# Optimization experiments

Measured on AMD Instinct MI355X. Metric: run time of the kernel, lower is better.

## Reference

```python
import jax, jax.numpy as jnp
import numpy as np

B, C, H, W = 2, 256, 64, 64  # C = in_channels; x has 2*C channels
DQ = C // 16


def setup_inputs() -> dict:
    key = jax.random.key(0)
    ks = jax.random.split(key, 10)
    s = 0.05
    return {
        "x": jax.random.normal(ks[0], (B, 2 * C, H, W), dtype=jnp.float32),
        "Wq": jax.random.normal(ks[1], (DQ, C), dtype=jnp.float32) * s,
        "bq": jax.random.normal(ks[2], (DQ,), dtype=jnp.float32) * s,
        "Wk": jax.random.normal(ks[3], (DQ, C), dtype=jnp.float32) * s,
        "bk": jax.random.normal(ks[4], (DQ,), dtype=jnp.float32) * s,
        "Wv": jax.random.normal(ks[5], (C, C), dtype=jnp.float32) * s,
        "bv": jax.random.normal(ks[6], (C,), dtype=jnp.float32) * s,
        "Wpt": jax.random.normal(ks[7], (C, 2 * C), dtype=jnp.float32) * s,
        "bpt": jax.random.normal(ks[8], (C,), dtype=jnp.float32) * s,
        "gamma": jnp.full((1,), 0.5, dtype=jnp.float32),  # original inits to 0; nonzero for a non-trivial output
    }


def _conv1x1(x, Wt, b):
    # 1x1 conv == per-pixel linear map over channels
    return jnp.einsum("bchw,dc->bdhw", x, Wt) + b[None, :, None, None]


def reference(x, Wq, bq, Wk, bk, Wv, bv, Wpt, bpt, gamma):
    n = x.shape[1] // 2
    x1, x2 = x[:, :n], x[:, n:]
    b, c, h, w = x1.shape
    hw = h * w

    def qkv(xi):
        q = _conv1x1(xi, Wq, bq).reshape(b, DQ, hw)   # [B,dq,HW]
        k = _conv1x1(xi, Wk, bk).reshape(b, DQ, hw)   # [B,dq,HW]
        v = _conv1x1(xi, Wv, bv).reshape(b, c, hw)    # [B,C,HW]
        return q, k, v

    q1, k1, v1 = qkv(x1)
    q2, k2, v2 = qkv(x2)

    # attn[b,i,j] = softmax_j( q[:,i] . k[:,j] )  (no scaling, as in original)
    attn1 = jax.nn.softmax(jnp.einsum("bdi,bdj->bij", q1, k1), axis=-1)  # [B,HW,HW]
    attn2 = jax.nn.softmax(jnp.einsum("bdi,bdj->bij", q2, k2), axis=-1)

    def apply_attn(v, attn):
        # out[b,c,i] = sum_j v[b,c,j] * attn[b,i,j]
        return jnp.einsum("bcj,bij->bci", v, attn).reshape(b, c, h, w)

    out11 = apply_attn(v1, attn1)
    out12 = apply_attn(v2, attn1)
    out21 = apply_attn(v1, attn2)
    out22 = apply_attn(v2, attn2)

    o1 = _conv1x1(jnp.concatenate([out11, out12], axis=1), Wpt, bpt)  # [B,C,H,W]
    o2 = _conv1x1(jnp.concatenate([out21, out22], axis=1), Wpt, bpt)

    out = gamma * jnp.concatenate([o1, o2], axis=1) + x
    return out
```

## Files before the change

### kernel.cpp

```cpp
#include <hip/hip_runtime.h>
#include <hip/hip_bf16.h>


#define HW 4096
#define CC 256
#define DQ 16

typedef __hip_bfloat16 bf16;
struct alignas(8) bh4 { bf16 x, y, z, w; };
typedef __bf16 bf16x8 __attribute__((ext_vector_type(8)));
typedef float  f32x4  __attribute__((ext_vector_type(4)));

static __device__ __forceinline__ float b2f(bf16 v) { return __bfloat162float(v); }
static __device__ __forceinline__ float ldf(const void* p, size_t i, bool isb) {
    return isb ? b2f(((const bf16*)p)[i]) : ((const float*)p)[i];
}

static __device__ __forceinline__ void load_lds16(const void* g, void* l) {
    __builtin_amdgcn_global_load_lds(
        (const __attribute__((address_space(1))) unsigned int*)g,
        (__attribute__((address_space(3))) unsigned int*)l, 16, 0, 0);
}

__global__ void __launch_bounds__(256)
prep_w(const void* __restrict__ Wq_r, const void* __restrict__ bq_r,
       const void* __restrict__ Wk_r, const void* __restrict__ bk_r,
       const void* __restrict__ Wv_r, const void* __restrict__ bv_r,
       const void* __restrict__ Wpt_r, const void* __restrict__ bpt_r,
       const void* __restrict__ gam_r,
       float* __restrict__ bqf, float* __restrict__ bkf, float* __restrict__ gamf,
       bf16* __restrict__ Wqb, bf16* __restrict__ Wkb,
       bf16* __restrict__ McB, float* __restrict__ btot,
       const unsigned short* __restrict__ probe) {
    int bx = blockIdx.x, tid = threadIdx.x;
    bool isb = probe[0] != 0;
    if (bx < 512) {
        int d = bx >> 1;
        int c = ((bx & 1) << 8) + tid;
        int half = c >> 8, cm = c & 255;
        size_t wp = (size_t)d * 512 + half * 256;
        float a0 = 0.f, a1 = 0.f, a2 = 0.f, a3 = 0.f;
        if (isb) {
            const bf16* Wp = (const bf16*)Wpt_r + wp;
            const bf16* Wv = (const bf16*)Wv_r + cm;
#pragma unroll 8
            for (int e = 0; e < 256; e += 4) {
                a0 = fmaf(b2f(Wp[e + 0]), b2f(Wv[(size_t)(e + 0) * 256]), a0);
                a1 = fmaf(b2f(Wp[e + 1]), b2f(Wv[(size_t)(e + 1) * 256]), a1);
                a2 = fmaf(b2f(Wp[e + 2]), b2f(Wv[(size_t)(e + 2) * 256]), a2);
                a3 = fmaf(b2f(Wp[e + 3]), b2f(Wv[(size_t)(e + 3) * 256]), a3);
            }
        } else {
            const float* Wp = (const float*)Wpt_r + wp;
            const float* Wv = (const float*)Wv_r + cm;
#pragma unroll 8
            for (int e = 0; e < 256; e += 4) {
                a0 = fmaf(Wp[e + 0], Wv[(size_t)(e + 0) * 256], a0);
                a1 = fmaf(Wp[e + 1], Wv[(size_t)(e + 1) * 256], a1);
                a2 = fmaf(Wp[e + 2], Wv[(size_t)(e + 2) * 256], a2);
                a3 = fmaf(Wp[e + 3], Wv[(size_t)(e + 3) * 256], a3);
            }
        }
        McB[d * 512 + c] = __float2bfloat16((a0 + a1) + (a2 + a3));
    } else if (bx == 512) {
        int d = tid;
        float a0 = 0.f, a1 = 0.f, a2 = 0.f, a3 = 0.f;
#pragma unroll 8
        for (int e = 0; e < 256; e += 4) {
            a0 = fmaf(ldf(Wpt_r, (size_t)d * 512 + e + 0, isb) + ldf(Wpt_r, (size_t)d * 512 + 256 + e + 0, isb), ldf(bv_r, e + 0, isb), a0);
            a1 = fmaf(ldf(Wpt_r, (size_t)d * 512 + e + 1, isb) + ldf(Wpt_r, (size_t)d * 512 + 256 + e + 1, isb), ldf(bv_r, e + 1, isb), a1);
            a2 = fmaf(ldf(Wpt_r, (size_t)d * 512 + e + 2, isb) + ldf(Wpt_r, (size_t)d * 512 + 256 + e + 2, isb), ldf(bv_r, e + 2, isb), a2);
            a3 = fmaf(ldf(Wpt_r, (size_t)d * 512 + e + 3, isb) + ldf(Wpt_r, (size_t)d * 512 + 256 + e + 3, isb), ldf(bv_r, e + 3, isb), a3);
        }
        btot[d] = ldf(bpt_r, d, isb) + ((a0 + a1) + (a2 + a3));
    } else if (bx < 545) {
        int id = bx - 513;
        const void* s = id < 16 ? Wq_r : Wk_r;
        bf16* dst = id < 16 ? Wqb : Wkb;
        int i = (id & 15) * 256 + tid;
        dst[i] = __float2bfloat16(ldf(s, i, isb));
    } else {
        if (tid < 16) bqf[tid] = ldf(bq_r, tid, isb);
        else if (tid < 32) bkf[tid - 16] = ldf(bk_r, tid - 16, isb);
        else if (tid == 32) gamf[0] = ldf(gam_r, 0, isb);
    }
}

__global__ void __launch_bounds__(256)
prep_x(const void* __restrict__ xsrc, bf16* __restrict__ Xt,
       const unsigned short* __restrict__ probe) {
    __shared__ float T[64][65];
    int id = blockIdx.x, tid = threadIdx.x;
    bool isb = probe[0] != 0;
    int j0 = (id & 63) * 64, e0 = ((id >> 6) & 7) * 64, b = id >> 9;
    int j_l = tid & 63, er0 = (tid >> 6) * 16;
#pragma unroll
    for (int r = 0; r < 16; ++r) {
        size_t src = ((size_t)(b * 512 + e0 + er0 + r)) * HW + j0 + j_l;
        T[er0 + r][j_l] = ldf(xsrc, src, isb);
    }
    __syncthreads();
    int e_w = tid & 63, jr0 = (tid >> 6) * 16;
#pragma unroll
    for (int r = 0; r < 16; ++r)
        Xt[((size_t)b * HW + j0 + jr0 + r) * 512 + e0 + e_w] =
            __float2bfloat16(T[e_w][jr0 + r]);
}

__global__ void __launch_bounds__(256, 2)
qku(const bf16* __restrict__ Xt,
    const bf16* __restrict__ Wqb, const float* __restrict__ bqf,
    const bf16* __restrict__ Wkb, const float* __restrict__ bkf,
    bf16* __restrict__ Qb, bf16* __restrict__ Kb,
    const bf16* __restrict__ McB, bf16* __restrict__ Ub) {
    __shared__ __align__(16) bf16 sA[64 * 64];
    __shared__ __align__(16) bf16 sB[128 * 64];
    int tid = threadIdx.x;
    int lane = tid & 63, wave = tid >> 6;
    int ln = lane & 15, q = lane >> 4;
    int bx = blockIdx.x;

    if (bx < 256) {
        int bh = bx >> 6;
        int b = bh >> 1, h = bh & 1;
        int j0 = (bx & 63) * 64 + wave * 16;
        bf16x8 aQ[8], aK[8];
#pragma unroll
        for (int kk = 0; kk < 8; ++kk) {
            aQ[kk] = *(const bf16x8*)&Wqb[ln * 256 + kk * 32 + q * 8];
            aK[kk] = *(const bf16x8*)&Wkb[ln * 256 + kk * 32 + q * 8];
        }
        const bf16* Xrow = Xt + ((size_t)b * HW + j0 + ln) * 512 + h * 256;
        f32x4 dQ = {0.f, 0.f, 0.f, 0.f}, dK = {0.f, 0.f, 0.f, 0.f};
#pragma unroll
        for (int kk = 0; kk < 8; ++kk) {
            bf16x8 bxv = *(const bf16x8*)&Xrow[kk * 32 + q * 8];
            dQ = __builtin_amdgcn_mfma_f32_16x16x32_bf16(aQ[kk], bxv, dQ, 0, 0, 0);
            dK = __builtin_amdgcn_mfma_f32_16x16x32_bf16(aK[kk], bxv, dK, 0, 0, 0);
        }
        size_t rowoff = ((size_t)bh * HW + j0 + ln) * 32;
        bh4 oq, ok;
        oq.x = __float2bfloat16(dQ[0] + bqf[q * 4 + 0]);
        oq.y = __float2bfloat16(dQ[1] + bqf[q * 4 + 1]);
        oq.z = __float2bfloat16(dQ[2] + bqf[q * 4 + 2]);
        oq.w = __float2bfloat16(dQ[3] + bqf[q * 4 + 3]);
        ok.x = __float2bfloat16(dK[0] + bkf[q * 4 + 0]);
        ok.y = __float2bfloat16(dK[1] + bkf[q * 4 + 1]);
        ok.z = __float2bfloat16(dK[2] + bkf[q * 4 + 2]);
        ok.w = __float2bfloat16(dK[3] + bkf[q * 4 + 3]);
        bh4 z; z.x = z.y = z.z = z.w = __float2bfloat16(0.f);
        *(bh4*)&Qb[rowoff + q * 4] = oq;
        *(bh4*)&Qb[rowoff + 16 + q * 4] = z;
        *(bh4*)&Kb[rowoff + q * 4] = ok;
        *(bh4*)&Kb[rowoff + 16 + q * 4] = z;
        return;
    }

    int id = bx - 256;
    int wm = (wave >> 1) * 32, wn = (wave & 1) * 64;
    int j0 = (id & 31) * 128, c0 = ((id >> 5) & 3) * 64, b = id >> 7;
    const bf16* Xb = Xt + (size_t)b * HW * 512;
    f32x4 acc[2][4];
#pragma unroll
    for (int mi = 0; mi < 2; ++mi)
#pragma unroll
        for (int ni = 0; ni < 4; ++ni)
#pragma unroll
            for (int r = 0; r < 4; ++r) acc[mi][ni][r] = 0.f;

    for (int e0 = 0; e0 < 512; e0 += 64) {
        __syncthreads();
#pragma unroll
        for (int r = 0; r < 2; ++r) {
            int s = r * 256 + tid;
            int row = s >> 3, jc = s & 7, jg = jc ^ (row & 7);
            load_lds16(McB + (size_t)(c0 + row) * 512 + e0 + jg * 8, sA + s * 8);
        }
#pragma unroll
        for (int r = 0; r < 4; ++r) {
            int s = r * 256 + tid;
            int row = s >> 3, jc = s & 7, jg = jc ^ (row & 7);
            load_lds16(Xb + (size_t)(j0 + row) * 512 + e0 + jg * 8, sB + s * 8);
        }
        __syncthreads();
#pragma unroll
        for (int kh = 0; kh < 2; ++kh) {
            bf16x8 af[2], bfv[4];
#pragma unroll
            for (int mi = 0; mi < 2; ++mi) {
                int row = wm + mi * 16 + ln;
                int jc = (kh * 4 + q) ^ (row & 7);
                af[mi] = *(const bf16x8*)&sA[row * 64 + jc * 8];
            }
#pragma unroll
            for (int ni = 0; ni < 4; ++ni) {
                int row = wn + ni * 16 + ln;
                int jc = (kh * 4 + q) ^ (row & 7);
                bfv[ni] = *(const bf16x8*)&sB[row * 64 + jc * 8];
            }
#pragma unroll
            for (int mi = 0; mi < 2; ++mi)
#pragma unroll
                for (int ni = 0; ni < 4; ++ni)
                    acc[mi][ni] = __builtin_amdgcn_mfma_f32_16x16x32_bf16(
                        af[mi], bfv[ni], acc[mi][ni], 0, 0, 0);
        }
    }
#pragma unroll
    for (int mi = 0; mi < 2; ++mi)
#pragma unroll
        for (int r = 0; r < 4; ++r) {
            int c = c0 + wm + mi * 16 + q * 4 + r;
#pragma unroll
            for (int ni = 0; ni < 4; ++ni) {
                int j = j0 + wn + ni * 16 + ln;
                Ub[((size_t)(b * CC + c)) * HW + j] = __float2bfloat16(acc[mi][ni][r]);
            }
        }
}

__global__ void __launch_bounds__(256, 4)
flash_attn(const bf16* __restrict__ Ub, const bf16* __restrict__ Qb,
           const bf16* __restrict__ Kb, const float* __restrict__ btot,
           const void* __restrict__ xorig, const float* __restrict__ gamf,
           void* __restrict__ outv, const unsigned short* __restrict__ probe) {
    __shared__ __align__(16) bf16 sU[2][128 * 64];
    __shared__ __align__(16) bf16 sE[32 * 64];
    __shared__ float sL[2][32];
    int tid  = threadIdx.x;
    int lane = tid & 63, wave = tid >> 6;
    int ln = lane & 15, q = lane >> 4;
    int iw = wave & 1, jw = wave >> 1;

    int bid = blockIdx.x;
    int panel = bid & 7;
    int i0 = (bid >> 3) * 32;
    int c0 = (panel & 1) * 128;
    int bh = panel >> 1;
    int b = bh >> 1, h = bh & 1;

    const bf16* Ubb = Ub + (size_t)b * CC * HW + (size_t)c0 * HW;
    const bf16* Kbh = Kb + (size_t)bh * HW * 32;

    bf16x8 bq = *(const bf16x8*)&Qb[((size_t)bh * HW + i0 + iw * 16 + ln) * 32 + q * 8];

    f32x4 acc[2][2];
#pragma unroll
    for (int mi = 0; mi < 2; ++mi)
#pragma unroll
        for (int ni = 0; ni < 2; ++ni)
#pragma unroll
            for (int r = 0; r < 4; ++r) acc[mi][ni][r] = 0.f;
    float lsum = 0.f;

    auto stage_u = [&](int tn, int bufn) {
#pragma unroll
        for (int r = 0; r < 4; ++r) {
            int s = r * 256 + tid;
            int row = s >> 3, jc = s & 7, jg = jc ^ (row & 7);
            load_lds16(Ubb + (size_t)row * HW + tn * 64 + jg * 8, &sU[bufn][s * 8]);
        }
    };
    auto load_k2 = [&](int tn, bf16x8 (&kf)[2]) {
#pragma unroll
        for (int s = 0; s < 2; ++s) {
            int js = jw * 2 + s;
            kf[s] = *(const bf16x8*)&Kbh[(size_t)(tn * 64 + js * 16 + ln) * 32 + q * 8];
        }
    };

    auto iter = [&](int t, bf16x8 (&kf_cur)[2], bf16x8 (&kf_nxt)[2]) {
        stage_u((t + 1) & 63, (t + 1) & 1);

#pragma unroll
        for (int s = 0; s < 2; ++s) {
            int js = jw * 2 + s;
            f32x4 d = {0.f, 0.f, 0.f, 0.f};
            d = __builtin_amdgcn_mfma_f32_16x16x32_bf16(kf_cur[s], bq, d, 0, 0, 0);
            float e0 = __expf(d[0]), e1 = __expf(d[1]);
            float e2 = __expf(d[2]), e3 = __expf(d[3]);
            lsum += (e0 + e1) + (e2 + e3);
            bh4 o;
            o.x = __float2bfloat16(e0);
            o.y = __float2bfloat16(e1);
            o.z = __float2bfloat16(e2);
            o.w = __float2bfloat16(e3);
            int row = iw * 16 + ln;
            int chunk = (js * 2 + (q >> 1)) ^ (row & 7);
            *(bh4*)&sE[row * 64 + chunk * 8 + (q & 1) * 4] = o;
        }

        load_k2((t + 1) & 63, kf_nxt);

        asm volatile("s_waitcnt lgkmcnt(0)" ::: "memory");
        __builtin_amdgcn_sched_barrier(0);
        __builtin_amdgcn_s_barrier();
        __builtin_amdgcn_sched_barrier(0);

        const bf16* sUc = sU[t & 1];
        __builtin_amdgcn_s_setprio(1);
#pragma unroll
        for (int kh = 0; kh < 2; ++kh) {
            bf16x8 bfv[2], af[2];
#pragma unroll
            for (int ni = 0; ni < 2; ++ni) {
                int row = ni * 16 + ln;
                int jc = (kh * 4 + q) ^ (row & 7);
                bfv[ni] = *(const bf16x8*)&sE[row * 64 + jc * 8];
            }
#pragma unroll
            for (int mi = 0; mi < 2; ++mi) {
                int row = wave * 32 + mi * 16 + ln;
                int jc = (kh * 4 + q) ^ (row & 7);
                af[mi] = *(const bf16x8*)&sUc[row * 64 + jc * 8];
            }
#pragma unroll
            for (int mi = 0; mi < 2; ++mi)
#pragma unroll
                for (int ni = 0; ni < 2; ++ni)
                    acc[mi][ni] = __builtin_amdgcn_mfma_f32_16x16x32_bf16(
                        af[mi], bfv[ni], acc[mi][ni], 0, 0, 0);
        }
        __builtin_amdgcn_s_setprio(0);

        asm volatile("s_waitcnt vmcnt(0) lgkmcnt(0)" ::: "memory");
        __builtin_amdgcn_sched_barrier(0);
        __builtin_amdgcn_s_barrier();
        __builtin_amdgcn_sched_barrier(0);
    };

    bf16x8 kfA[2], kfB[2];
    load_k2(0, kfA);
    stage_u(0, 0);
    asm volatile("s_waitcnt vmcnt(0)" ::: "memory");
    __builtin_amdgcn_sched_barrier(0);
    __builtin_amdgcn_s_barrier();
    __builtin_amdgcn_sched_barrier(0);

    for (int tt = 0; tt < 64; tt += 2) {
        iter(tt, kfA, kfB);
        iter(tt + 1, kfB, kfA);
    }

    lsum += __shfl_xor(lsum, 16);
    lsum += __shfl_xor(lsum, 32);
    if (lane < 16) sL[jw][iw * 16 + lane] = lsum;
    __syncthreads();

    bool isb = probe[0] != 0;
    float g = gamf[0];
    float lv[2];
#pragma unroll
    for (int ni = 0; ni < 2; ++ni)
        lv[ni] = 1.f / (sL[0][ni * 16 + ln] + sL[1][ni * 16 + ln]);
#pragma unroll
    for (int mi = 0; mi < 2; ++mi)
#pragma unroll
        for (int r = 0; r < 4; ++r) {
            int c = c0 + wave * 32 + mi * 16 + q * 4 + r;
            float bt = btot[c];
            size_t rowbase = ((size_t)(b * 512 + h * 256 + c)) * HW + i0;
#pragma unroll
            for (int ni = 0; ni < 2; ++ni) {
                size_t idx = rowbase + ni * 16 + ln;
                float xres = isb ? b2f(((const bf16*)xorig)[idx]) : ((const float*)xorig)[idx];
                float o = fmaf(g, fmaf(acc[mi][ni][r], lv[ni], bt), xres);
                if (isb) ((bf16*)outv)[idx] = __float2bfloat16(o);
                else     ((float*)outv)[idx] = o;
            }
        }
}

extern "C" void kernel_launch(void* const* d_in, const int* in_sizes, int n_in,
                              void* d_out, int out_size, void* d_ws, size_t ws_size,
                              hipStream_t stream) {
    const unsigned short* probe = (const unsigned short*)d_in[9];

    char* ws = (char*)d_ws;
    size_t off = 0;
    auto alloc = [&](size_t bytes) { size_t r = off; off = (off + bytes + 255) & ~(size_t)255; return r; };
    float* bqf  = (float*)(ws + alloc(16 * 4));
    float* bkf  = (float*)(ws + alloc(16 * 4));
    float* gamf = (float*)(ws + alloc(4));
    bf16*  Xt   = (bf16*)(ws + alloc((size_t)2 * HW * 512 * 2));
    bf16*  McB  = (bf16*)(ws + alloc(256 * 512 * 2));
    float* btot = (float*)(ws + alloc(256 * 4));
    bf16*  Wqb  = (bf16*)(ws + alloc(DQ * 256 * 2));
    bf16*  Wkb  = (bf16*)(ws + alloc(DQ * 256 * 2));
    bf16*  Qb   = (bf16*)(ws + alloc((size_t)4 * HW * 32 * 2));
    bf16*  Kb   = (bf16*)(ws + alloc((size_t)4 * HW * 32 * 2));
    bf16*  Ub   = (bf16*)(ws + alloc((size_t)2 * CC * HW * 2));

    prep_w<<<dim3(546), 256, 0, stream>>>(
        d_in[1], d_in[2], d_in[3], d_in[4], d_in[5], d_in[6],
        d_in[7], d_in[8], d_in[9],
        bqf, bkf, gamf, Wqb, Wkb, McB, btot, probe);

    prep_x<<<dim3(1024), 256, 0, stream>>>(d_in[0], Xt, probe);

    qku<<<dim3(512), 256, 0, stream>>>(Xt, Wqb, bqf, Wkb, bkf, Qb, Kb, McB, Ub);

    flash_attn<<<dim3(1024), 256, 0, stream>>>(Ub, Qb, Kb, btot, d_in[0], gamf, d_out, probe);
}
```

Baseline: 242.3 us.

## Compute fused Wpt·Wv weight product with MFMA inside prep_x

The scalar per-thread 256-long dot products that formed the combined projection weight McB in prep_w are replaced. prep_w now only converts Wpt to bf16 and writes a transposed bf16 Wv. Eight extra blocks appended to prep_x then compute McB with bf16 MFMA 16x16x32 instructions, so the weight fusion overlaps with the x transpose. This removes slow strided scalar loads, but rounds the Wpt and Wv inputs to bf16 before the product and adds workspace buffers.

```diff
diff --git a/kernel.cpp b/kernel.cpp
--- a/kernel.cpp
+++ b/kernel.cpp
@@ -30,39 +30,40 @@
        const void* __restrict__ gam_r,
        float* __restrict__ bqf, float* __restrict__ bkf, float* __restrict__ gamf,
        bf16* __restrict__ Wqb, bf16* __restrict__ Wkb,
-       bf16* __restrict__ McB, float* __restrict__ btot,
+       bf16* __restrict__ Wptb, bf16* __restrict__ WvTb, float* __restrict__ btot,
        const unsigned short* __restrict__ probe) {
+    __shared__ float T[64][65];
     int bx = blockIdx.x, tid = threadIdx.x;
     bool isb = probe[0] != 0;
-    if (bx < 512) {
-        int d = bx >> 1;
-        int c = ((bx & 1) << 8) + tid;
-        int half = c >> 8, cm = c & 255;
-        size_t wp = (size_t)d * 512 + half * 256;
-        float a0 = 0.f, a1 = 0.f, a2 = 0.f, a3 = 0.f;
-        if (isb) {
-            const bf16* Wp = (const bf16*)Wpt_r + wp;
-            const bf16* Wv = (const bf16*)Wv_r + cm;
-#pragma unroll 8
-            for (int e = 0; e < 256; e += 4) {
-                a0 = fmaf(b2f(Wp[e + 0]), b2f(Wv[(size_t)(e + 0) * 256]), a0);
-                a1 = fmaf(b2f(Wp[e + 1]), b2f(Wv[(size_t)(e + 1) * 256]), a1);
-                a2 = fmaf(b2f(Wp[e + 2]), b2f(Wv[(size_t)(e + 2) * 256]), a2);
-                a3 = fmaf(b2f(Wp[e + 3]), b2f(Wv[(size_t)(e + 3) * 256]), a3);
-            }
-        } else {
-            const float* Wp = (const float*)Wpt_r + wp;
-            const float* Wv = (const float*)Wv_r + cm;
-#pragma unroll 8
-            for (int e = 0; e < 256; e += 4) {
-                a0 = fmaf(Wp[e + 0], Wv[(size_t)(e + 0) * 256], a0);
-                a1 = fmaf(Wp[e + 1], Wv[(size_t)(e + 1) * 256], a1);
-                a2 = fmaf(Wp[e + 2], Wv[(size_t)(e + 2) * 256], a2);
-                a3 = fmaf(Wp[e + 3], Wv[(size_t)(e + 3) * 256], a3);
-            }
-        }
-        McB[d * 512 + c] = __float2bfloat16((a0 + a1) + (a2 + a3));
-    } else if (bx == 512) {
+    if (bx < 64) {
+        size_t base = (size_t)bx * 2048 + tid * 8;
+#pragma unroll
+        for (int r = 0; r < 8; ++r)
+            Wptb[base + r] = __float2bfloat16(ldf(Wpt_r, base + r, isb));
+    } else if (bx < 80) {
+        int id = bx - 64;
+        int e0 = (id >> 2) * 64, c0 = (id & 3) * 64;
+        int c_l = tid & 63, er0 = (tid >> 6) * 16;
+#pragma unroll
+        for (int r = 0; r < 16; ++r)
+            T[er0 + r][c_l] = ldf(Wv_r, (size_t)(e0 + er0 + r) * 256 + c0 + c_l, isb);
+        __syncthreads();
+        int e_w = tid & 63, cr0 = (tid >> 6) * 16;
+#pragma unroll
+        for (int r = 0; r < 16; ++r)
+            WvTb[(size_t)(c0 + cr0 + r) * 256 + e0 + e_w] =
+                __float2bfloat16(T[e_w][cr0 + r]);
+    } else if (bx < 96) {
+        int i = (bx - 80) * 256 + tid;
+        Wqb[i] = __float2bfloat16(ldf(Wq_r, i, isb));
+    } else if (bx < 112) {
+        int i = (bx - 96) * 256 + tid;
+        Wkb[i] = __float2bfloat16(ldf(Wk_r, i, isb));
+    } else if (bx == 112) {
+        if (tid < 16) bqf[tid] = ldf(bq_r, tid, isb);
+        else if (tid < 32) bkf[tid - 16] = ldf(bk_r, tid - 16, isb);
+        else if (tid == 32) gamf[0] = ldf(gam_r, 0, isb);
+    } else {
         int d = tid;
         float a0 = 0.f, a1 = 0.f, a2 = 0.f, a3 = 0.f;
 #pragma unroll 8
@@ -73,38 +74,60 @@
             a3 = fmaf(ldf(Wpt_r, (size_t)d * 512 + e + 3, isb) + ldf(Wpt_r, (size_t)d * 512 + 256 + e + 3, isb), ldf(bv_r, e + 3, isb), a3);
         }
         btot[d] = ldf(bpt_r, d, isb) + ((a0 + a1) + (a2 + a3));
-    } else if (bx < 545) {
-        int id = bx - 513;
-        const void* s = id < 16 ? Wq_r : Wk_r;
-        bf16* dst = id < 16 ? Wqb : Wkb;
-        int i = (id & 15) * 256 + tid;
-        dst[i] = __float2bfloat16(ldf(s, i, isb));
-    } else {
-        if (tid < 16) bqf[tid] = ldf(bq_r, tid, isb);
-        else if (tid < 32) bkf[tid - 16] = ldf(bk_r, tid - 16, isb);
-        else if (tid == 32) gamf[0] = ldf(gam_r, 0, isb);
     }
 }
 
 __global__ void __launch_bounds__(256)
 prep_x(const void* __restrict__ xsrc, bf16* __restrict__ Xt,
+       const bf16* __restrict__ Wptb, const bf16* __restrict__ WvTb,
+       bf16* __restrict__ McB,
        const unsigned short* __restrict__ probe) {
     __shared__ float T[64][65];
-    int id = blockIdx.x, tid = threadIdx.x;
-    bool isb = probe[0] != 0;
-    int j0 = (id & 63) * 64, e0 = ((id >> 6) & 7) * 64, b = id >> 9;
-    int j_l = tid & 63, er0 = (tid >> 6) * 16;
-#pragma unroll
-    for (int r = 0; r < 16; ++r) {
-        size_t src = ((size_t)(b * 512 + e0 + er0 + r)) * HW + j0 + j_l;
-        T[er0 + r][j_l] = ldf(xsrc, src, isb);
-    }
-    __syncthreads();
-    int e_w = tid & 63, jr0 = (tid >> 6) * 16;
-#pragma unroll
-    for (int r = 0; r < 16; ++r)
-        Xt[((size_t)b * HW + j0 + jr0 + r) * 512 + e0 + e_w] =
-            __float2bfloat16(T[e_w][jr0 + r]);
+    int bx = blockIdx.x, tid = threadIdx.x;
+    if (bx < 1024) {
+        bool isb = probe[0] != 0;
+        int j0 = (bx & 63) * 64, e0 = ((bx >> 6) & 7) * 64, b = bx >> 9;
+        int j_l = tid & 63, er0 = (tid >> 6) * 16;
+#pragma unroll
+        for (int r = 0; r < 16; ++r) {
+            size_t src = ((size_t)(b * 512 + e0 + er0 + r)) * HW + j0 + j_l;
+            T[er0 + r][j_l] = ldf(xsrc, src, isb);
+        }
+        __syncthreads();
+        int e_w = tid & 63, jr0 = (tid >> 6) * 16;
+#pragma unroll
+        for (int r = 0; r < 16; ++r)
+            Xt[((size_t)b * HW + j0 + jr0 + r) * 512 + e0 + e_w] =
+                __float2bfloat16(T[e_w][jr0 + r]);
+        return;
+    }
+    int m = bx - 1024;
+    int half = m & 1, dq = m >> 1;
+    int lane = tid & 63, wave = tid >> 6;
+    int ln = lane & 15, q = lane >> 4;
+    int d0 = dq * 64 + wave * 16;
+
+    f32x4 acc[16];
+#pragma unroll
+    for (int c = 0; c < 16; ++c)
+#pragma unroll
+        for (int r = 0; r < 4; ++r) acc[c][r] = 0.f;
+
+#pragma unroll
+    for (int kk = 0; kk < 8; ++kk) {
+        bf16x8 a = *(const bf16x8*)&Wptb[(size_t)(d0 + ln) * 512 + half * 256 + kk * 32 + q * 8];
+#pragma unroll
+        for (int c = 0; c < 16; ++c) {
+            bf16x8 bv = *(const bf16x8*)&WvTb[(size_t)(c * 16 + ln) * 256 + kk * 32 + q * 8];
+            acc[c] = __builtin_amdgcn_mfma_f32_16x16x32_bf16(a, bv, acc[c], 0, 0, 0);
+        }
+    }
+#pragma unroll
+    for (int c = 0; c < 16; ++c)
+#pragma unroll
+        for (int r = 0; r < 4; ++r)
+            McB[(size_t)(d0 + q * 4 + r) * 512 + half * 256 + c * 16 + ln] =
+                __float2bfloat16(acc[c][r]);
 }
 
 __global__ void __launch_bounds__(256, 2)
@@ -390,13 +413,15 @@
     bf16*  Qb   = (bf16*)(ws + alloc((size_t)4 * HW * 32 * 2));
     bf16*  Kb   = (bf16*)(ws + alloc((size_t)4 * HW * 32 * 2));
     bf16*  Ub   = (bf16*)(ws + alloc((size_t)2 * CC * HW * 2));
-
-    prep_w<<<dim3(546), 256, 0, stream>>>(
+    bf16*  Wptb = (bf16*)(ws + alloc(256 * 512 * 2));
+    bf16*  WvTb = (bf16*)(ws + alloc(256 * 256 * 2));
+
+    prep_w<<<dim3(114), 256, 0, stream>>>(
         d_in[1], d_in[2], d_in[3], d_in[4], d_in[5], d_in[6],
         d_in[7], d_in[8], d_in[9],
-        bqf, bkf, gamf, Wqb, Wkb, McB, btot, probe);
-
-    prep_x<<<dim3(1024), 256, 0, stream>>>(d_in[0], Xt, probe);
+        bqf, bkf, gamf, Wqb, Wkb, Wptb, WvTb, btot, probe);
+
+    prep_x<<<dim3(1032), 256, 0, stream>>>(d_in[0], Xt, Wptb, WvTb, McB, probe);
 
     qku<<<dim3(512), 256, 0, stream>>>(Xt, Wqb, bqf, Wkb, bkf, Qb, Kb, McB, Ub);
 
```

Measured after the change: 257.4 us. +6.2%, slower.
